# Kernel tuning notes

Measured on AMD Instinct MI355X. Metric: run time of the kernel, lower is better.

## Reference

```python
import jax, jax.numpy as jnp
import numpy as np

B, N, F, E, D = 2, 50000, 128, 800000, 4


def setup_inputs() -> dict:
    key = jax.random.key(0)
    ks = jax.random.split(key, 6)
    X = jax.random.normal(ks[0], (B, N, F), dtype=jnp.float32)
    u_val = jax.random.normal(ks[1], (E, D), dtype=jnp.float32)
    u_rows = jax.random.randint(ks[2], (E,), 0, N, dtype=jnp.int32)
    u_cols = jax.random.randint(ks[3], (E,), 0, N, dtype=jnp.int32)
    mu = jax.random.uniform(ks[4], (1, D), minval=-0.05, maxval=0.05, dtype=jnp.float32)
    # sigma kept away from 0 so sigma^2 in the denominator is numerically sane
    sigma = jax.random.uniform(ks[5], (1, D), minval=0.5, maxval=1.5, dtype=jnp.float32)
    return {"X": X, "u_val": u_val, "u_rows": u_rows, "u_cols": u_cols,
            "mu": mu, "sigma": sigma, "u_shape": N}


def reference(X, u_val, u_rows, u_cols, mu, sigma, u_shape):
    n = u_shape  # python int, static
    # per-edge Gaussian kernel log-weight: -0.5 * sum_d (u-mu)^2 / (sigma^2+eps)
    w = -0.5 * jnp.sum(jnp.square(u_val - mu) / (jnp.square(sigma) + 1e-14), axis=1)  # [E]
    # sparse (segment) softmax over rows == tf.sparse.softmax on reordered SparseTensor
    m = jax.ops.segment_max(w, u_rows, num_segments=n)          # [N]
    e = jnp.exp(w - m[u_rows])                                  # [E]
    s = jax.ops.segment_sum(e, u_rows, num_segments=n)          # [N]
    sm = e / s[u_rows]                                          # [E]
    # sparse-dense matmul: D[b,i,f] = sum_{edges e: row=i} sm_e * X[b, col_e, f]
    Xt = jnp.transpose(X, (1, 0, 2))                            # [N,B,F]
    msg = sm[:, None, None] * Xt[u_cols]                        # [E,B,F]
    Dn = jax.ops.segment_sum(msg, u_rows, num_segments=n)       # [N,B,F]
    return jnp.transpose(Dn, (1, 0, 2))                         # [B,N,F]
```

## Files before the change

### kernel.cpp

```cpp
#include <hip/hip_runtime.h>

constexpr int Bc = 2;
constexpr int Fc = 128;
constexpr int F4 = Fc / 4;
constexpr int ROWS_PER_BLOCK = 4;
constexpr int EPT = 8;
constexpr int BIN_EDGES = 256 * EPT;

typedef float vfloat4 __attribute__((ext_vector_type(4)));

__device__ __forceinline__ unsigned short f2bf(float f) {
    unsigned u = __float_as_uint(f);
    unsigned r = (u + 0x7FFFu + ((u >> 16) & 1u)) >> 16;
    return (unsigned short)r;
}
__device__ __forceinline__ float bf2f(unsigned short h) {
    return __uint_as_float(((unsigned)h) << 16);
}
__device__ __forceinline__ void nt_store4(float4 v, float4* p) {
    vfloat4 q = {v.x, v.y, v.z, v.w};
    __builtin_nontemporal_store(q, (vfloat4*)p);
}

__global__ __launch_bounds__(256) void prep_kernel(const float4* __restrict__ uval,
                                                   const float* __restrict__ mu,
                                                   const float* __restrict__ sigma,
                                                   const int* __restrict__ rows,
                                                   const int* __restrict__ cols,
                                                   int2* __restrict__ bucket_buf,
                                                   int* __restrict__ bucket_cursor,
                                                   const float4* __restrict__ X4,
                                                   ushort4* __restrict__ Xb,
                                                   int E, int N, int cap, int nbuk,
                                                   int nbin) {
    __shared__ int hist[256];
    __shared__ int excl[256];
    __shared__ int fill[256];
    __shared__ int chunkb[256];
    __shared__ int sh[256];
    __shared__ int2 staged[BIN_EDGES];

    int t = threadIdx.x;

    if (blockIdx.x >= nbin) {
        long idx = (long)(blockIdx.x - nbin) * 256 + t;
        long tot = (long)Bc * N * F4;
        if (idx < tot) {
            int b  = (int)(idx / ((long)N * F4));
            int nt_ = (int)(idx - (long)b * N * F4);
            int n  = nt_ >> 5;
            int f4 = nt_ & 31;
            float4 v = X4[(size_t)b * N * F4 + nt_];
            ushort4 o;
            o.x = f2bf(v.x); o.y = f2bf(v.y); o.z = f2bf(v.z); o.w = f2bf(v.w);
            Xb[(size_t)n * (Bc * F4) + b * F4 + f4] = o;
        }
        return;
    }

    hist[t] = 0;
    float m0 = mu[0], m1 = mu[1], m2 = mu[2], m3 = mu[3];
    float i0 = 1.0f / (sigma[0] * sigma[0] + 1e-14f);
    float i1 = 1.0f / (sigma[1] * sigma[1] + 1e-14f);
    float i2 = 1.0f / (sigma[2] * sigma[2] + 1e-14f);
    float i3 = 1.0f / (sigma[3] * sigma[3] + 1e-14f);
    __syncthreads();

    int e0 = blockIdx.x * BIN_EDGES;
    int meta_r[EPT];
    float ev_r[EPT];
    int buk_r[EPT];
    #pragma unroll
    for (int it = 0; it < EPT; ++it) {
        int e = e0 + it * 256 + t;
        if (e < E) {
            int r = rows[e];
            int c = cols[e];
            float4 u = uval[e];
            float d0 = u.x - m0, d1 = u.y - m1, d2 = u.z - m2, d3 = u.w - m3;
            float w = -0.5f * (d0 * d0 * i0 + d1 * d1 * i1 + d2 * d2 * i2 + d3 * d3 * i3);
            ev_r[it]   = expf(w);
            meta_r[it] = (r << 16) | c;
            buk_r[it]  = r >> 8;
            atomicAdd(&hist[buk_r[it]], 1);
        } else {
            buk_r[it] = -1;
        }
    }
    __syncthreads();

    int v = hist[t];
    sh[t] = v;
    __syncthreads();
    for (int off = 1; off < 256; off <<= 1) {
        int a = (t >= off) ? sh[t - off] : 0;
        __syncthreads();
        sh[t] += a;
        __syncthreads();
    }
    excl[t] = sh[t] - v;
    fill[t] = sh[t] - v;

    if (t < nbuk && v > 0) chunkb[t] = atomicAdd(&bucket_cursor[t], v);
    __syncthreads();

    #pragma unroll
    for (int it = 0; it < EPT; ++it) {
        if (buk_r[it] >= 0) {
            int rk = atomicAdd(&fill[buk_r[it]], 1);
            staged[rk] = make_int2(meta_r[it], __float_as_int(ev_r[it]));
        }
    }
    __syncthreads();

    int nst = min(BIN_EDGES, E - e0);
    for (int k = t; k < nst; k += 256) {
        int2 x = staged[k];
        int buk = ((unsigned)x.x) >> 24;
        int rel = chunkb[buk] + (k - excl[buk]);
        if (rel < cap)
            bucket_buf[(size_t)buk * cap + rel] = x;
    }
}

__global__ __launch_bounds__(256) void csr_kernel(const int2* __restrict__ bucket_buf,
                                                  const int* __restrict__ bucket_cursor,
                                                  int2* __restrict__ pairs,
                                                  int* __restrict__ rowstart,
                                                  int cap, int N, int nbuk) {
    __shared__ int hist[256];
    __shared__ int excl[256];
    __shared__ int cur[256];
    __shared__ int sh[256];
    int b = blockIdx.x;
    int t = threadIdx.x;

    int szt = (t < nbuk) ? min(bucket_cursor[t], cap) : 0;
    sh[t] = szt;
    __syncthreads();
    for (int off = 1; off < 256; off <<= 1) {
        int a = (t >= off) ? sh[t - off] : 0;
        __syncthreads();
        sh[t] += a;
        __syncthreads();
    }
    int cbase = (b == 0) ? 0 : sh[b - 1];
    int size  = min(bucket_cursor[b], cap);
    if (b == nbuk - 1 && t == 0) rowstart[N] = sh[nbuk - 1];
    __syncthreads();

    hist[t] = 0;
    __syncthreads();
    int base = b * cap;
    for (int k = t; k < size; k += 256) {
        unsigned m = (unsigned)bucket_buf[base + k].x;
        atomicAdd(&hist[(m >> 16) & 0xFF], 1);
    }
    __syncthreads();
    int v = hist[t];
    sh[t] = v;
    __syncthreads();
    for (int off = 1; off < 256; off <<= 1) {
        int a = (t >= off) ? sh[t - off] : 0;
        __syncthreads();
        sh[t] += a;
        __syncthreads();
    }
    excl[t] = sh[t] - v;
    cur[t]  = sh[t] - v;
    int row = b * 256 + t;
    if (row < N) rowstart[row] = cbase + excl[t];
    __syncthreads();
    for (int k = t; k < size; k += 256) {
        int2 x = bucket_buf[base + k];
        unsigned m = (unsigned)x.x;
        int rk = atomicAdd(&cur[(m >> 16) & 0xFF], 1);
        pairs[cbase + rk] = make_int2((int)(m & 0xFFFFu), x.y);
    }
}

__global__ __launch_bounds__(256) void spmm_bf16(const ushort4* __restrict__ Xb,
                                                 const int2* __restrict__ pairs,
                                                 const int* __restrict__ rowstart,
                                                 float4* __restrict__ out4, int N) {
    int lane = threadIdx.x & 63;
    int i = blockIdx.x * ROWS_PER_BLOCK + (threadIdx.x >> 6);
    if (i >= N) return;
    int start = rowstart[i];
    int end   = rowstart[i + 1];
    int len   = end - start;
    float4 acc = {0.f, 0.f, 0.f, 0.f};
    float sum = 0.f;
    for (int c = 0; c < len; c += 64) {
        int m = min(64, len - c);
        int2 myp = make_int2(0, 0);
        if (lane < m) myp = pairs[start + c + lane];
        for (int g = 0; g < m; g += 8) {
            int   colv[8];
            float evv[8];
            #pragma unroll
            for (int e = 0; e < 8; ++e) {
                colv[e] = __shfl(myp.x, g + e);
                evv[e]  = __int_as_float(__shfl(myp.y, g + e));
            }
            ushort4 xs[8];
            #pragma unroll
            for (int e = 0; e < 8; ++e)
                xs[e] = Xb[(size_t)colv[e] * 64 + lane];
            #pragma unroll
            for (int e = 0; e < 8; ++e) {
                float ev = evv[e];
                sum += ev;
                acc.x = fmaf(ev, bf2f(xs[e].x), acc.x);
                acc.y = fmaf(ev, bf2f(xs[e].y), acc.y);
                acc.z = fmaf(ev, bf2f(xs[e].z), acc.z);
                acc.w = fmaf(ev, bf2f(xs[e].w), acc.w);
            }
        }
    }
    if (len > 0) {
        float inv = 1.0f / sum;
        acc.x *= inv; acc.y *= inv; acc.z *= inv; acc.w *= inv;
    }
    int b  = lane >> 5;
    int f4 = lane & 31;
    nt_store4(acc, &out4[(size_t)b * N * F4 + (size_t)i * F4 + f4]);
}

__global__ __launch_bounds__(256) void spmm_f32(const float4* __restrict__ X4,
                                                const int2* __restrict__ pairs,
                                                const int* __restrict__ rowstart,
                                                float4* __restrict__ out4, int N) {
    int lane = threadIdx.x & 63;
    int i = blockIdx.x * ROWS_PER_BLOCK + (threadIdx.x >> 6);
    if (i >= N) return;
    int start = rowstart[i];
    int end   = rowstart[i + 1];
    int b  = lane >> 5;
    int f4 = lane & 31;
    float4 acc = {0.f, 0.f, 0.f, 0.f};
    float sum = 0.f;
    if (start < end) {
        int xbase = b * N * F4 + f4;
        for (int j = start; j < end; ++j) {
            int2 p = pairs[j];
            float ev = __int_as_float(p.y);
            sum += ev;
            float4 x = X4[xbase + (size_t)p.x * F4];
            acc.x = fmaf(ev, x.x, acc.x);
            acc.y = fmaf(ev, x.y, acc.y);
            acc.z = fmaf(ev, x.z, acc.z);
            acc.w = fmaf(ev, x.w, acc.w);
        }
        float inv = 1.0f / sum;
        acc.x *= inv; acc.y *= inv; acc.z *= inv; acc.w *= inv;
    }
    nt_store4(acc, &out4[(size_t)b * N * F4 + (size_t)i * F4 + f4]);
}

extern "C" void kernel_launch(void* const* d_in, const int* in_sizes, int n_in,
                              void* d_out, int out_size, void* d_ws, size_t ws_size,
                              hipStream_t stream) {
    const float* X      = (const float*)d_in[0];
    const float* u_val  = (const float*)d_in[1];
    const int*   u_rows = (const int*)d_in[2];
    const int*   u_cols = (const int*)d_in[3];
    const float* mu     = (const float*)d_in[4];
    const float* sigma  = (const float*)d_in[5];

    const int E = in_sizes[2];
    const int N = in_sizes[0] / (Bc * Fc);
    const int nbuk = (N + 255) >> 8;

    size_t off = 0;
    auto carve = [&](size_t bytes) -> char* {
        char* p = (char*)d_ws + off;
        off = (off + bytes + 255) & ~(size_t)255;
        return p;
    };
    int*  bucket_cursor = (int*)carve(256 * 4);
    int*  rowstart      = (int*)carve((size_t)(N + 1) * 4);
    int2* pairs         = (int2*)carve((size_t)E * 8);

    size_t xb_bytes = (size_t)N * Bc * Fc * 2;
    size_t avail    = (ws_size > off) ? (ws_size - off) : 0;
    int cap = 6144;
    size_t buck_bytes = (size_t)nbuk * cap * 8;
    if (buck_bytes + 512 > avail) {
        cap = (int)((avail - 512) / ((size_t)nbuk * 8));
        buck_bytes = (size_t)nbuk * cap * 8;
    }
    int2* bucket_buf = (int2*)carve(buck_bytes);
    bool use_bf16 = (off + xb_bytes) <= ws_size;
    ushort4* Xb = use_bf16 ? (ushort4*)carve(xb_bytes) : nullptr;

    hipMemsetAsync(bucket_cursor, 0, 256 * 4, stream);

    const int nbin  = (E + BIN_EDGES - 1) / BIN_EDGES;
    const int nconv = use_bf16 ? (int)(((long)Bc * N * F4 + 255) / 256) : 0;
    prep_kernel<<<nbin + nconv, 256, 0, stream>>>(
        (const float4*)u_val, mu, sigma, u_rows, u_cols,
        bucket_buf, bucket_cursor, (const float4*)X, Xb,
        E, N, cap, nbuk, nbin);
    csr_kernel<<<nbuk, 256, 0, stream>>>(bucket_buf, bucket_cursor,
                                         pairs, rowstart, cap, N, nbuk);
    if (use_bf16) {
        spmm_bf16<<<(N + ROWS_PER_BLOCK - 1) / ROWS_PER_BLOCK, 256, 0, stream>>>(
            Xb, pairs, rowstart, (float4*)d_out, N);
    } else {
        spmm_f32<<<(N + ROWS_PER_BLOCK - 1) / ROWS_PER_BLOCK, 256, 0, stream>>>(
            (const float4*)X, pairs, rowstart, (float4*)d_out, N);
    }
}
```

Measured before the change: 100.1 us.

## Speed up CSR build with wave-shuffle scans, 1024-thread blocks and LDS-staged scatter

Replaces the shared-memory Hillis-Steele scans in prep and csr kernels with wave-level shuffle scans plus a small cross-wave sum. The CSR kernel now runs 1024 threads per bucket, stages the row-sorted pairs in LDS and then writes them to global memory contiguously instead of scattering. It also adds nontemporal loads for the X conversion and u_val reads. The intent is to cut barrier count and uncoalesced writes in the small CSR stage. The cost is a larger LDS footprint (CAP_MAX int2 per block), which may reduce occupancy.

New measurement: 97.26 us. 1.03x faster.

```diff
diff --git a/kernel.cpp b/kernel.cpp
--- a/kernel.cpp
+++ b/kernel.cpp
@@ -6,6 +6,7 @@
 constexpr int ROWS_PER_BLOCK = 4;
 constexpr int EPT = 8;
 constexpr int BIN_EDGES = 256 * EPT;
+constexpr int CAP_MAX = 6144;
 
 typedef float vfloat4 __attribute__((ext_vector_type(4)));
 
@@ -20,6 +21,26 @@
 __device__ __forceinline__ void nt_store4(float4 v, float4* p) {
     vfloat4 q = {v.x, v.y, v.z, v.w};
     __builtin_nontemporal_store(q, (vfloat4*)p);
+}
+__device__ __forceinline__ float4 nt_load4(const float4* p) {
+    vfloat4 q = __builtin_nontemporal_load((const vfloat4*)p);
+    float4 r; r.x = q.x; r.y = q.y; r.z = q.z; r.w = q.w;
+    return r;
+}
+
+__device__ __forceinline__ int block_incl_scan256(int v, int* wsum, int t) {
+    int lane = t & 63, w = t >> 6;
+    #pragma unroll
+    for (int d = 1; d < 64; d <<= 1) {
+        int u = __shfl_up(v, d);
+        if (lane >= d) v += u;
+    }
+    if (lane == 63) wsum[w] = v;
+    __syncthreads();
+    int add = 0;
+    #pragma unroll
+    for (int i = 0; i < 3; ++i) if (i < w) add += wsum[i];
+    return v + add;
 }
 
 __global__ __launch_bounds__(256) void prep_kernel(const float4* __restrict__ uval,
@@ -37,7 +58,7 @@
     __shared__ int excl[256];
     __shared__ int fill[256];
     __shared__ int chunkb[256];
-    __shared__ int sh[256];
+    __shared__ int wsum[4];
     __shared__ int2 staged[BIN_EDGES];
 
     int t = threadIdx.x;
@@ -50,7 +71,7 @@
             int nt_ = (int)(idx - (long)b * N * F4);
             int n  = nt_ >> 5;
             int f4 = nt_ & 31;
-            float4 v = X4[(size_t)b * N * F4 + nt_];
+            float4 v = nt_load4(&X4[(size_t)b * N * F4 + nt_]);
             ushort4 o;
             o.x = f2bf(v.x); o.y = f2bf(v.y); o.z = f2bf(v.z); o.w = f2bf(v.w);
             Xb[(size_t)n * (Bc * F4) + b * F4 + f4] = o;
@@ -76,7 +97,7 @@
         if (e < E) {
             int r = rows[e];
             int c = cols[e];
-            float4 u = uval[e];
+            float4 u = nt_load4((const float4*)&uval[e]);
             float d0 = u.x - m0, d1 = u.y - m1, d2 = u.z - m2, d3 = u.w - m3;
             float w = -0.5f * (d0 * d0 * i0 + d1 * d1 * i1 + d2 * d2 * i2 + d3 * d3 * i3);
             ev_r[it]   = expf(w);
@@ -90,17 +111,10 @@
     __syncthreads();
 
     int v = hist[t];
-    sh[t] = v;
-    __syncthreads();
-    for (int off = 1; off < 256; off <<= 1) {
-        int a = (t >= off) ? sh[t - off] : 0;
-        __syncthreads();
-        sh[t] += a;
-        __syncthreads();
-    }
-    excl[t] = sh[t] - v;
-    fill[t] = sh[t] - v;
-
+    int incl = block_incl_scan256(v, wsum, t);
+    int ex = incl - v;
+    excl[t] = ex;
+    fill[t] = ex;
     if (t < nbuk && v > 0) chunkb[t] = atomicAdd(&bucket_cursor[t], v);
     __syncthreads();
 
@@ -123,60 +137,83 @@
     }
 }
 
-__global__ __launch_bounds__(256) void csr_kernel(const int2* __restrict__ bucket_buf,
-                                                  const int* __restrict__ bucket_cursor,
-                                                  int2* __restrict__ pairs,
-                                                  int* __restrict__ rowstart,
-                                                  int cap, int N, int nbuk) {
-    __shared__ int hist[256];
-    __shared__ int excl[256];
+__global__ __launch_bounds__(1024) void csr_kernel(const int2* __restrict__ bucket_buf,
+                                                   const int* __restrict__ bucket_cursor,
+                                                   int2* __restrict__ pairs,
+                                                   int* __restrict__ rowstart,
+                                                   int cap, int N, int nbuk) {
+    __shared__ int sh[256];
     __shared__ int cur[256];
-    __shared__ int sh[256];
+    __shared__ int wsum[4];
+    __shared__ int2 staged[CAP_MAX];
     int b = blockIdx.x;
     int t = threadIdx.x;
-
-    int szt = (t < nbuk) ? min(bucket_cursor[t], cap) : 0;
-    sh[t] = szt;
-    __syncthreads();
-    for (int off = 1; off < 256; off <<= 1) {
-        int a = (t >= off) ? sh[t - off] : 0;
-        __syncthreads();
-        sh[t] += a;
-        __syncthreads();
-    }
+    int lane = t & 63, w = t >> 6;
+
+    int vA = 0, sA = 0;
+    if (t < 256) {
+        vA = (t < nbuk) ? min(bucket_cursor[t], cap) : 0;
+        sA = vA;
+        #pragma unroll
+        for (int d = 1; d < 64; d <<= 1) {
+            int u = __shfl_up(sA, d);
+            if (lane >= d) sA += u;
+        }
+        if (lane == 63) wsum[w] = sA;
+    }
+    __syncthreads();
+    if (t < 256) {
+        int add = 0;
+        #pragma unroll
+        for (int i = 0; i < 3; ++i) if (i < w) add += wsum[i];
+        sh[t] = sA + add;
+    }
+    __syncthreads();
     int cbase = (b == 0) ? 0 : sh[b - 1];
     int size  = min(bucket_cursor[b], cap);
-    if (b == nbuk - 1 && t == 0) rowstart[N] = sh[nbuk - 1];
-    __syncthreads();
-
-    hist[t] = 0;
+    if (b == 0 && t == 0) rowstart[N] = sh[nbuk - 1];
+    __syncthreads();
+
+    if (t < 256) cur[t] = 0;
     __syncthreads();
     int base = b * cap;
-    for (int k = t; k < size; k += 256) {
+    for (int k = t; k < size; k += 1024) {
         unsigned m = (unsigned)bucket_buf[base + k].x;
-        atomicAdd(&hist[(m >> 16) & 0xFF], 1);
-    }
-    __syncthreads();
-    int v = hist[t];
-    sh[t] = v;
-    __syncthreads();
-    for (int off = 1; off < 256; off <<= 1) {
-        int a = (t >= off) ? sh[t - off] : 0;
-        __syncthreads();
-        sh[t] += a;
-        __syncthreads();
-    }
-    excl[t] = sh[t] - v;
-    cur[t]  = sh[t] - v;
-    int row = b * 256 + t;
-    if (row < N) rowstart[row] = cbase + excl[t];
-    __syncthreads();
-    for (int k = t; k < size; k += 256) {
+        atomicAdd(&cur[(m >> 16) & 0xFF], 1);
+    }
+    __syncthreads();
+
+    int vC = 0, sC = 0;
+    if (t < 256) {
+        vC = cur[t];
+        sC = vC;
+        #pragma unroll
+        for (int d = 1; d < 64; d <<= 1) {
+            int u = __shfl_up(sC, d);
+            if (lane >= d) sC += u;
+        }
+        if (lane == 63) wsum[w] = sC;
+    }
+    __syncthreads();
+    if (t < 256) {
+        int add = 0;
+        #pragma unroll
+        for (int i = 0; i < 3; ++i) if (i < w) add += wsum[i];
+        int ex = sC + add - vC;
+        cur[t] = ex;
+        int row = b * 256 + t;
+        if (row < N) rowstart[row] = cbase + ex;
+    }
+    __syncthreads();
+
+    for (int k = t; k < size; k += 1024) {
         int2 x = bucket_buf[base + k];
         unsigned m = (unsigned)x.x;
         int rk = atomicAdd(&cur[(m >> 16) & 0xFF], 1);
-        pairs[cbase + rk] = make_int2((int)(m & 0xFFFFu), x.y);
-    }
+        staged[rk] = make_int2((int)(m & 0xFFFFu), x.y);
+    }
+    __syncthreads();
+    for (int k = t; k < size; k += 1024) pairs[cbase + k] = staged[k];
 }
 
 __global__ __launch_bounds__(256) void spmm_bf16(const ushort4* __restrict__ Xb,
@@ -284,7 +321,7 @@
 
     size_t xb_bytes = (size_t)N * Bc * Fc * 2;
     size_t avail    = (ws_size > off) ? (ws_size - off) : 0;
-    int cap = 6144;
+    int cap = CAP_MAX;
     size_t buck_bytes = (size_t)nbuk * cap * 8;
     if (buck_bytes + 512 > avail) {
         cap = (int)((avail - 512) / ((size_t)nbuk * 8));
@@ -302,8 +339,8 @@
         (const float4*)u_val, mu, sigma, u_rows, u_cols,
         bucket_buf, bucket_cursor, (const float4*)X, Xb,
         E, N, cap, nbuk, nbin);
-    csr_kernel<<<nbuk, 256, 0, stream>>>(bucket_buf, bucket_cursor,
-                                         pairs, rowstart, cap, N, nbuk);
+    csr_kernel<<<nbuk, 1024, 0, stream>>>(bucket_buf, bucket_cursor,
+                                          pairs, rowstart, cap, N, nbuk);
     if (use_bf16) {
         spmm_bf16<<<(N + ROWS_PER_BLOCK - 1) / ROWS_PER_BLOCK, 256, 0, stream>>>(
             Xb, pairs, rowstart, (float4*)d_out, N);
```
